# Kernel tuning notes

Hardware: AMD Instinct MI355X
Metric: run time of the kernel (lower is better)

The kernel has to match this reference:

```python
import jax, jax.numpy as jnp
import numpy as np

IN_BW = 4
W_BW = 4
EPS = 1e-5


def quantize(x, bw):
    # k-bit uniform quantizer on [-1, 1 - 2^(1-bw)] with straight-through rounding
    scale = 2.0 ** (bw - 1)
    xc = jnp.clip(x, -1.0, 1.0 - 1.0 / scale)
    q = jnp.round(xc * scale) / scale
    return xc + jax.lax.stop_gradient(q - xc)


def bconv(x, w, stride):
    # BinarizeConv2d: quantize activations (in_bw) and weights (weight_bw), then conv
    return jax.lax.conv_general_dilated(
        quantize(x, IN_BW), quantize(w, W_BW),
        window_strides=stride, padding='VALID',
        dimension_numbers=('NCHW', 'OIHW', 'NCHW'))


def bn2d(x, g, b):
    mean = x.mean(axis=(0, 2, 3), keepdims=True)
    var = x.var(axis=(0, 2, 3), keepdims=True)
    return (x - mean) * jax.lax.rsqrt(var + EPS) * g.reshape(1, -1, 1, 1) + b.reshape(1, -1, 1, 1)


def bn1d(x, g, b):
    mean = x.mean(axis=0, keepdims=True)
    var = x.var(axis=0, keepdims=True)
    return (x - mean) * jax.lax.rsqrt(var + EPS) * g + b


def htanh(x):
    return jnp.clip(x, -1.0, 1.0)


def setup_inputs() -> dict:
    key = jax.random.key(0)
    ks = jax.random.split(key, 24)
    B = 8192
    d = {'x': jax.random.normal(ks[0], (B, 1, 1250, 1), dtype=jnp.float32)}
    # conv weights OIHW
    shapes = [(3, 1, 6, 1), (5, 3, 5, 1), (10, 5, 4, 1), (20, 10, 4, 1), (20, 20, 4, 1)]
    for i, s in enumerate(shapes):
        d[f'w{i+1}'] = 0.3 * jax.random.normal(ks[1 + i], s, dtype=jnp.float32)
    d['fw1'] = 0.3 * jax.random.normal(ks[6], (10, 740), dtype=jnp.float32)
    d['fw2'] = 0.3 * jax.random.normal(ks[7], (2, 10), dtype=jnp.float32)
    chans = [3, 5, 10, 20, 20, 10, 2]
    for i, c in enumerate(chans):
        d[f'g{i+1}'] = 1.0 + 0.1 * jax.random.normal(ks[8 + i], (c,), dtype=jnp.float32)
        d[f'b{i+1}'] = 0.1 * jax.random.normal(ks[15 + i], (c,), dtype=jnp.float32)
    return d


def reference(x, w1, w2, w3, w4, w5, fw1, fw2,
              g1, g2, g3, g4, g5, g6, g7,
              b1, b2, b3, b4, b5, b6, b7):
    h = htanh(bn2d(bconv(x, w1, (2, 1)), g1, b1))
    h = htanh(bn2d(bconv(h, w2, (2, 1)), g2, b2))
    h = htanh(bn2d(bconv(h, w3, (2, 1)), g3, b3))
    h = htanh(bn2d(bconv(h, w4, (2, 1)), g4, b4))
    h = htanh(bn2d(bconv(h, w5, (2, 1)), g5, b5))
    h = h.reshape(h.shape[0], -1)  # (B, 20*37*1) = (B, 740)
    # dropout is identity in eval mode
    h = htanh(bn1d(quantize(h, IN_BW) @ quantize(fw1, W_BW).T, g6, b6))
    h = bn1d(quantize(h, IN_BW) @ quantize(fw2, W_BW).T, g7, b7)
    return h
```

## Files before the change

kernel.cpp:

```cpp
#include <hip/hip_runtime.h>

#define DEV __device__ __forceinline__

DEV float qwt(float w) {
    float y = fminf(fmaxf(w, -1.0f), 0.875f);
    return rintf(y * 8.0f) * 0.125f;
}
DEV int qw8i(float w) {
    float y = fminf(fmaxf(w, -1.0f), 0.875f);
    return (int)rintf(y * 8.0f);
}
DEV int q8i(float x, float a, float b) {
    float y = fmaf(x, a, b);
    y = fminf(fmaxf(y, -1.0f), 0.875f);
    return (int)rintf(y * 8.0f);
}
DEV float qact(float x, float a, float b) {
    float y = fmaf(x, a, b);
    y = fminf(fmaxf(y, -1.0f), 0.875f);
    return rintf(y * 8.0f) * 0.125f;
}

DEV int dot4(int a, int b, int c) {
#if __has_builtin(__builtin_amdgcn_sdot4)
    return __builtin_amdgcn_sdot4(a, b, c, false);
#else
    c += (int)(signed char)(a)       * (int)(signed char)(b);
    c += (int)(signed char)(a >> 8)  * (int)(signed char)(b >> 8);
    c += (int)(signed char)(a >> 16) * (int)(signed char)(b >> 16);
    c += (int)(signed char)(a >> 24) * (int)(signed char)(b >> 24);
    return c;
#endif
}
DEV unsigned alignpair(unsigned hi, unsigned lo, int bits) {
#if __has_builtin(__builtin_amdgcn_alignbit)
    return __builtin_amdgcn_alignbit(hi, lo, bits);
#else
    return bits ? ((lo >> bits) | (hi << (32 - bits))) : lo;
#endif
}

DEV void pack_layer(const float* w, int* o, int CIN, int COUT, int K, int t) {
    int KW = (K + 3) / 4;
    for (int i = t; i < COUT * CIN * KW; i += 256) {
        int j = i % KW, cc = i / KW;
        unsigned r = 0;
        for (int u = 0; u < 4; u++) {
            int k = 4 * j + u;
            int b = (k < K) ? (qw8i(w[cc * K + k]) & 0xff) : 0;
            r |= (unsigned)b << (8 * u);
        }
        o[i] = (int)r;
    }
}
__global__ __launch_bounds__(256) void pack_k(
    const float* w1, const float* w2, const float* w3, const float* w4, const float* w5,
    int* o1, int* o2, int* o3, int* o4, int* o5)
{
    int t = threadIdx.x;
    pack_layer(w1, o1, 1, 3, 6, t);
    pack_layer(w2, o2, 3, 5, 5, t);
    pack_layer(w3, o3, 5, 10, 4, t);
    pack_layer(w4, o4, 10, 20, 4, t);
    pack_layer(w5, o5, 20, 20, 4, t);
}

template<int CIN,int COUT,int K,int LINP,int LOUT,int LOUTP,int P,int R,bool IN_FLOAT,int LIN=0>
__global__ __launch_bounds__(256) void conv_k(
    const void* __restrict__ in_, const int* __restrict__ wqi,
    const float* __restrict__ tr, short* __restrict__ out,
    float* __restrict__ partial, int B)
{
    constexpr int KW   = (K + 3) / 4;
    constexpr int NE   = P + 2 * KW - 1;
    constexpr int ND   = (2 * (NE - 1) + 3) / 4 + 2;
    constexpr int LO_P = (LOUT + P - 1) / P;
    constexpr int GROUPS = R * LO_P;

    __shared__ __align__(16) signed char smem[R * CIN * LINP + 32];
    __shared__ float ts[CIN > 0 ? CIN : 1], tb[CIN > 0 ? CIN : 1];
    __shared__ float red[4][2 * COUT];

    const int tid = threadIdx.x;

    if constexpr (!IN_FLOAT) {
        if (tid < CIN) {
            ts[tid] = tr[tid] * 0.015625f;
            tb[tid] = tr[CIN + tid];
        }
        __syncthreads();
    }

    const int r0   = blockIdx.x * R;
    const int rcnt = min(R, B - r0);

    if constexpr (IN_FLOAT) {
        constexpr int CH = LIN / 2;
        const float2* gp = (const float2*)in_;
        for (int c = tid; c < rcnt * CH; c += 256) {
            int r = c / CH, rem = c - r * CH;
            float2 v = gp[(size_t)(r0 + r) * CH + rem];
            int b0 = q8i(v.x, 1.f, 0.f) & 0xff;
            int b1 = q8i(v.y, 1.f, 0.f) & 0xff;
            *(unsigned short*)(smem + r * LINP + rem * 2) =
                (unsigned short)(b0 | (b1 << 8));
        }
    } else {
        constexpr int CH  = CIN * LINP / 8;
        constexpr int CHC = LINP / 8;
        const int4* gp = (const int4*)((const short*)in_ + (size_t)r0 * CIN * LINP);
        for (int c = tid; c < rcnt * CH; c += 256) {
            int rem = c % CH;
            int ci = rem / CHC;
            float a = ts[ci], bo = tb[ci];
            int4 v = gp[c];
            int vs[4] = { v.x, v.y, v.z, v.w };
            unsigned pk[2];
#pragma unroll
            for (int u = 0; u < 2; u++) {
                unsigned pp = 0;
#pragma unroll
                for (int j = 0; j < 2; j++) {
                    int word = vs[u * 2 + j];
                    int b0 = q8i((float)(short)(word & 0xffff), a, bo) & 0xff;
                    int b1 = q8i((float)(short)(word >> 16),    a, bo) & 0xff;
                    pp |= (unsigned)(b0 | (b1 << 8)) << (16 * j);
                }
                pk[u] = pp;
            }
            ((uint2*)smem)[c] = make_uint2(pk[0], pk[1]);
        }
    }
    __syncthreads();

    float tsum[COUT], tsq[COUT];
#pragma unroll
    for (int c = 0; c < COUT; c++) { tsum[c] = 0.f; tsq[c] = 0.f; }

#pragma unroll 1
    for (int g = tid; g < GROUPS; g += 256) {
        int r = g / LO_P;
        if (r >= rcnt) continue;
        int l0   = (g - r * LO_P) * P;
        int pact = min(P, LOUT - l0);

        int acc[COUT][P];
#pragma unroll
        for (int co = 0; co < COUT; co++)
#pragma unroll
            for (int p = 0; p < P; p++) acc[co][p] = 0;

        const int ibase = r * CIN * LINP + 2 * l0;
        const int sh    = (P % 2 == 0) ? 0 : (ibase & 3);

        for (int ci = 0; ci < CIN; ci++) {
            const int* sp = (const int*)smem + ((ci * LINP + (ibase & ~3)) >> 2);
            int d[ND];
#pragma unroll
            for (int j = 0; j < ND; j++) d[j] = sp[j];
            int e[NE];
#pragma unroll
            for (int i = 0; i < NE; i++) {
                int off = sh + 2 * i;
                e[i] = (int)alignpair((unsigned)d[off / 4 + 1], (unsigned)d[off / 4], (off & 3) * 8);
            }
#pragma unroll
            for (int co = 0; co < COUT; co++) {
#pragma unroll
                for (int j = 0; j < KW; j++) {
                    int wv = wqi[(co * CIN + ci) * KW + j];
#pragma unroll
                    for (int p = 0; p < P; p++)
                        acc[co][p] = dot4(e[p + 2 * j], wv, acc[co][p]);
                }
            }
        }

        const size_t ob = (size_t)(r0 + r) * COUT * LOUTP + l0;
#pragma unroll
        for (int co = 0; co < COUT; co++) {
            if (pact == P) {
                short tmp[P];
#pragma unroll
                for (int p = 0; p < P; p++) {
                    tmp[p] = (short)acc[co][p];
                    float v = (float)acc[co][p] * 0.015625f;
                    tsum[co] += v;
                    tsq[co]   = fmaf(v, v, tsq[co]);
                }
                short* op = &out[ob + (size_t)co * LOUTP];
                if constexpr (P == 1) {
                    op[0] = tmp[0];
                } else if constexpr (P == 2) {
                    *(short2*)op = make_short2(tmp[0], tmp[1]);
                } else if constexpr (P == 4) {
                    *(short4*)op = make_short4(tmp[0], tmp[1], tmp[2], tmp[3]);
                } else if constexpr (P == 8) {
                    *(short4*)op       = make_short4(tmp[0], tmp[1], tmp[2], tmp[3]);
                    *(short4*)(op + 4) = make_short4(tmp[4], tmp[5], tmp[6], tmp[7]);
                }
            } else {
#pragma unroll
                for (int p = 0; p < P; p++) {
                    if (p < pact) {
                        out[ob + (size_t)co * LOUTP + p] = (short)acc[co][p];
                        float v = (float)acc[co][p] * 0.015625f;
                        tsum[co] += v;
                        tsq[co]   = fmaf(v, v, tsq[co]);
                    }
                }
            }
        }
    }

    const int lane = tid & 63, wid = tid >> 6;
#pragma unroll
    for (int co = 0; co < COUT; co++) {
        float s = tsum[co], q = tsq[co];
        for (int off = 32; off > 0; off >>= 1) {
            s += __shfl_down(s, off, 64);
            q += __shfl_down(q, off, 64);
        }
        if (lane == 0) { red[wid][2 * co] = s; red[wid][2 * co + 1] = q; }
    }
    __syncthreads();
    if (tid < 2 * COUT) {
        float v = red[0][tid] + red[1][tid] + red[2][tid] + red[3][tid];
        partial[(size_t)blockIdx.x * (2 * COUT) + tid] = v;
    }
}

__global__ __launch_bounds__(256) void finalize_k(
    const float* __restrict__ partial, int G, int C, double N,
    const float* __restrict__ gamma, const float* __restrict__ beta,
    float* __restrict__ trout)
{
    const int c = blockIdx.x;
    double s = 0.0, q = 0.0;
    for (int g = threadIdx.x; g < G; g += 256) {
        s += (double)partial[(size_t)g * 2 * C + 2 * c];
        q += (double)partial[(size_t)g * 2 * C + 2 * c + 1];
    }
    for (int off = 32; off > 0; off >>= 1) {
        s += __shfl_down(s, off, 64);
        q += __shfl_down(q, off, 64);
    }
    __shared__ double rs[4], rq[4];
    int lane = threadIdx.x & 63, wid = threadIdx.x >> 6;
    if (lane == 0) { rs[wid] = s; rq[wid] = q; }
    __syncthreads();
    if (threadIdx.x == 0) {
        double S = rs[0] + rs[1] + rs[2] + rs[3];
        double Q = rq[0] + rq[1] + rq[2] + rq[3];
        double mean = S / N;
        double var  = Q / N - mean * mean;
        double inv  = 1.0 / sqrt(var + 1e-5);
        double sc   = (double)gamma[c] * inv;
        trout[c]     = (float)sc;
        trout[C + c] = (float)((double)beta[c] - mean * sc);
    }
}

__global__ __launch_bounds__(256) void fc1_k(
    const short* __restrict__ y5, const float* __restrict__ fw1,
    const float* __restrict__ tr, float* __restrict__ z1,
    float* __restrict__ partial, int B)
{
    __shared__ float wq[7400];
    __shared__ float ts[20], tb[20];
    __shared__ float red[4][20];
    const int tid = threadIdx.x;
    for (int i = tid; i < 7400; i += 256) wq[i] = qwt(fw1[i]);
    if (tid < 20) { ts[tid] = tr[tid]; tb[tid] = tr[20 + tid]; }
    __syncthreads();

    const int lane = tid & 63, wid = tid >> 6;
    float tsum[10], tsq[10];
#pragma unroll
    for (int j = 0; j < 10; j++) { tsum[j] = 0.f; tsq[j] = 0.f; }

#pragma unroll 1
    for (int r = blockIdx.x * 4 + wid; r < B; r += gridDim.x * 4) {
        const short* xr = y5 + (size_t)r * 800;
        float acc[10];
#pragma unroll
        for (int j = 0; j < 10; j++) acc[j] = 0.f;
#pragma unroll 1
        for (int f = lane; f < 740; f += 64) {
            int c = f / 37, pos = f - c * 37;
            float x = qact((float)xr[c * 40 + pos] * 0.015625f, ts[c], tb[c]);
#pragma unroll
            for (int j = 0; j < 10; j++) acc[j] = fmaf(x, wq[j * 740 + f], acc[j]);
        }
#pragma unroll
        for (int j = 0; j < 10; j++) {
            float v = acc[j];
            for (int off = 1; off < 64; off <<= 1) v += __shfl_xor(v, off, 64);
            tsum[j] += v; tsq[j] = fmaf(v, v, tsq[j]);
            if (lane == j) z1[(size_t)r * 10 + j] = v;
        }
    }
    if (lane == 0) {
#pragma unroll
        for (int j = 0; j < 10; j++) { red[wid][2 * j] = tsum[j]; red[wid][2 * j + 1] = tsq[j]; }
    }
    __syncthreads();
    if (tid < 20) {
        float v = red[0][tid] + red[1][tid] + red[2][tid] + red[3][tid];
        partial[(size_t)blockIdx.x * 20 + tid] = v;
    }
}

__global__ __launch_bounds__(256) void fc2_fused_k(
    const float* __restrict__ z1, const float* __restrict__ fw2,
    const float* __restrict__ part6, int G6,
    const float* __restrict__ g6, const float* __restrict__ b6,
    const float* __restrict__ g7, const float* __restrict__ b7,
    float* __restrict__ outp, int B)
{
    __shared__ float zbuf[16384];
    __shared__ double dred[4][20];
    __shared__ double dtot[20];
    __shared__ float ts7[10], tb7[10], wq2[20];
    __shared__ float fr[4][4];
    __shared__ float tr8[4];

    const int tid = threadIdx.x;
    const int lane = tid & 63, wid = tid >> 6;

    double ls[20];
#pragma unroll
    for (int c = 0; c < 20; c++) ls[c] = 0.0;
    for (int g = tid; g < G6; g += 256) {
#pragma unroll
        for (int c = 0; c < 20; c++) ls[c] += (double)part6[(size_t)g * 20 + c];
    }
#pragma unroll
    for (int c = 0; c < 20; c++) {
        double v = ls[c];
        for (int off = 32; off > 0; off >>= 1) v += __shfl_down(v, off, 64);
        if (lane == 0) dred[wid][c] = v;
    }
    if (tid < 20) wq2[tid] = qwt(fw2[tid]);
    __syncthreads();
    if (tid < 20) dtot[tid] = dred[0][tid] + dred[1][tid] + dred[2][tid] + dred[3][tid];
    __syncthreads();
    if (tid < 10) {
        double N = (double)B;
        double mean = dtot[2 * tid] / N;
        double var  = dtot[2 * tid + 1] / N - mean * mean;
        double inv  = 1.0 / sqrt(var + 1e-5);
        double sc   = (double)g6[tid] * inv;
        ts7[tid] = (float)sc;
        tb7[tid] = (float)((double)b6[tid] - mean * sc);
    }
    __syncthreads();

    float s0 = 0.f, q0 = 0.f, s1 = 0.f, q1 = 0.f;
#pragma unroll 1
    for (int r = tid; r < B; r += 256) {
        float a0 = 0.f, a1 = 0.f;
#pragma unroll
        for (int i = 0; i < 10; i++) {
            float x = qact(z1[(size_t)r * 10 + i], ts7[i], tb7[i]);
            a0 = fmaf(x, wq2[i], a0);
            a1 = fmaf(x, wq2[10 + i], a1);
        }
        zbuf[r * 2]     = a0;
        zbuf[r * 2 + 1] = a1;
        s0 += a0; q0 = fmaf(a0, a0, q0);
        s1 += a1; q1 = fmaf(a1, a1, q1);
    }
    for (int off = 32; off > 0; off >>= 1) {
        s0 += __shfl_down(s0, off, 64); q0 += __shfl_down(q0, off, 64);
        s1 += __shfl_down(s1, off, 64); q1 += __shfl_down(q1, off, 64);
    }
    if (lane == 0) { fr[wid][0] = s0; fr[wid][1] = q0; fr[wid][2] = s1; fr[wid][3] = q1; }
    __syncthreads();
    if (tid < 2) {
        double S = 0.0, Q = 0.0;
        for (int w = 0; w < 4; w++) { S += (double)fr[w][2 * tid]; Q += (double)fr[w][2 * tid + 1]; }
        double N = (double)B;
        double mean = S / N;
        double var  = Q / N - mean * mean;
        double inv  = 1.0 / sqrt(var + 1e-5);
        double sc   = (double)g7[tid] * inv;
        tr8[tid]     = (float)sc;
        tr8[2 + tid] = (float)((double)b7[tid] - mean * sc);
    }
    __syncthreads();
    for (int i = tid; i < 2 * B; i += 256) {
        int c = i & 1;
        outp[i] = fmaf(zbuf[i], tr8[c], tr8[2 + c]);
    }
}

extern "C" void kernel_launch(void* const* d_in, const int* in_sizes, int n_in,
                              void* d_out, int out_size, void* d_ws, size_t ws_size,
                              hipStream_t stream)
{
    const float* x   = (const float*)d_in[0];
    const float* w1  = (const float*)d_in[1];
    const float* w2  = (const float*)d_in[2];
    const float* w3  = (const float*)d_in[3];
    const float* w4  = (const float*)d_in[4];
    const float* w5  = (const float*)d_in[5];
    const float* fw1 = (const float*)d_in[6];
    const float* fw2 = (const float*)d_in[7];
    const float *g[7], *bb[7];
    for (int i = 0; i < 7; i++) { g[i] = (const float*)d_in[8 + 2 * i]; bb[i] = (const float*)d_in[9 + 2 * i]; }

    char* ws = (char*)d_ws;
    size_t off = 0;
    auto alloc = [&](size_t bytes) -> void* {
        void* q = ws + off;
        off += (bytes + 255) & ~(size_t)255;
        return q;
    };
    short* y1 = (short*)alloc((size_t)8192 * 3 * 624 * 2);
    short* y2 = (short*)alloc((size_t)8192 * 5 * 312 * 2);
    short* y3 = (short*)alloc((size_t)8192 * 10 * 160 * 2);
    short* y4 = (short*)alloc((size_t)8192 * 20 * 80 * 2);
    short* y5 = (short*)alloc((size_t)8192 * 20 * 40 * 2);
    float* z1 = (float*)alloc((size_t)81920 * 4);
    float* partial = (float*)alloc((size_t)81920 * 4);
    int*   wp1 = (int*)alloc(64);   int* wp2 = (int*)alloc(256);
    int*   wp3 = (int*)alloc(256);  int* wp4 = (int*)alloc(1024);
    int*   wp5 = (int*)alloc(2048);
    float* tr2 = (float*)alloc(256); float* tr3 = (float*)alloc(256);
    float* tr4 = (float*)alloc(256); float* tr5 = (float*)alloc(256);
    float* tr6 = (float*)alloc(256); float* tr7 = (float*)alloc(256);

    const int B = 8192;

    pack_k<<<1, 256, 0, stream>>>(w1, w2, w3, w4, w5, wp1, wp2, wp3, wp4, wp5);

    {
        int grid = (B + 2) / 3;
        conv_k<1, 3, 6, 1252, 623, 624, 8, 3, true, 1250>
            <<<grid, 256, 0, stream>>>(x, wp1, nullptr, y1, partial, B);
        finalize_k<<<3, 256, 0, stream>>>(partial, grid, 3, (double)B * 623.0, g[0], bb[0], tr2);
    }
    {
        int grid = B / 4;
        conv_k<3, 5, 5, 624, 310, 312, 4, 4, false>
            <<<grid, 256, 0, stream>>>(y1, wp2, tr2, y2, partial, B);
        finalize_k<<<5, 256, 0, stream>>>(partial, grid, 5, (double)B * 310.0, g[1], bb[1], tr3);
    }
    {
        int grid = B / 4;
        conv_k<5, 10, 4, 312, 154, 160, 2, 4, false>
            <<<grid, 256, 0, stream>>>(y2, wp3, tr3, y3, partial, B);
        finalize_k<<<10, 256, 0, stream>>>(partial, grid, 10, (double)B * 154.0, g[2], bb[2], tr4);
    }
    {
        int grid = B / 4;
        conv_k<10, 20, 4, 160, 76, 80, 1, 4, false>
            <<<grid, 256, 0, stream>>>(y3, wp4, tr4, y4, partial, B);
        finalize_k<<<20, 256, 0, stream>>>(partial, grid, 20, (double)B * 76.0, g[3], bb[3], tr5);
    }
    {
        int grid = B / 8;
        conv_k<20, 20, 4, 80, 37, 40, 1, 8, false>
            <<<grid, 256, 0, stream>>>(y4, wp5, tr5, y5, partial, B);
        finalize_k<<<20, 256, 0, stream>>>(partial, grid, 20, (double)B * 37.0, g[4], bb[4], tr6);
    }
    {
        int grid = 2048;
        fc1_k<<<grid, 256, 0, stream>>>(y5, fw1, tr6, z1, partial, B);
        fc2_fused_k<<<1, 256, 0, stream>>>(z1, fw2, partial, grid,
                                           g[5], bb[5], g[6], bb[6],
                                           (float*)d_out, B);
    }
}
```

Measured before the change: 303.7 us.

## Fold BN stat finalization and weight packing into consumer kernels via integer atomics

Removes the separate finalize_k launches and the pack_k launch. Each conv or fc kernel now accumulates exact integer sums and sums of squares and adds them with 64-bit atomics into 64 slot buffers. The next kernel reduces those slots itself and computes the BN scale and shift at block start. The first conv packs its own weights into shared memory, and its block 0 packs the weights for the later layers. This cuts kernel launches and serial gaps, at the cost of atomics, a memset, and a small redundant stat reduction in every block.

```diff
diff --git a/kernel.cpp b/kernel.cpp
--- a/kernel.cpp
+++ b/kernel.cpp
@@ -39,6 +39,11 @@
     return bits ? ((lo >> bits) | (hi << (32 - bits))) : lo;
 #endif
 }
+DEV long long shfl_down_ll(long long v, int off) {
+    int lo = __shfl_down((int)(v & 0xffffffffll), off, 64);
+    int hi = __shfl_down((int)(v >> 32), off, 64);
+    return ((long long)hi << 32) | (unsigned)lo;
+}
 
 DEV void pack_layer(const float* w, int* o, int CIN, int COUT, int K, int t) {
     int KW = (K + 3) / 4;
@@ -53,23 +58,19 @@
         o[i] = (int)r;
     }
 }
-__global__ __launch_bounds__(256) void pack_k(
-    const float* w1, const float* w2, const float* w3, const float* w4, const float* w5,
-    int* o1, int* o2, int* o3, int* o4, int* o5)
-{
-    int t = threadIdx.x;
-    pack_layer(w1, o1, 1, 3, 6, t);
-    pack_layer(w2, o2, 3, 5, 5, t);
-    pack_layer(w3, o3, 5, 10, 4, t);
-    pack_layer(w4, o4, 10, 20, 4, t);
-    pack_layer(w5, o5, 20, 20, 4, t);
-}
 
 template<int CIN,int COUT,int K,int LINP,int LOUT,int LOUTP,int P,int R,bool IN_FLOAT,int LIN=0>
 __global__ __launch_bounds__(256) void conv_k(
     const void* __restrict__ in_, const int* __restrict__ wqi,
-    const float* __restrict__ tr, short* __restrict__ out,
-    float* __restrict__ partial, int B)
+    const long long* __restrict__ statsIn,
+    const float* __restrict__ gprev, const float* __restrict__ bprev,
+    double Nprev,
+    short* __restrict__ out, long long* __restrict__ statsOut, int B,
+    const float* __restrict__ wown,
+    const float* __restrict__ pw2, const float* __restrict__ pw3,
+    const float* __restrict__ pw4, const float* __restrict__ pw5,
+    int* __restrict__ owp2, int* __restrict__ owp3,
+    int* __restrict__ owp4, int* __restrict__ owp5)
 {
     constexpr int KW   = (K + 3) / 4;
     constexpr int NE   = P + 2 * KW - 1;
@@ -78,20 +79,60 @@
     constexpr int GROUPS = R * LO_P;
 
     __shared__ __align__(16) signed char smem[R * CIN * LINP + 32];
-    __shared__ float ts[CIN > 0 ? CIN : 1], tb[CIN > 0 ? CIN : 1];
-    __shared__ float red[4][2 * COUT];
+    __shared__ long long lred[2 * CIN * 16];
+    __shared__ long long redll[4][2 * COUT];
+    __shared__ float ts[CIN], tb[CIN];
+    __shared__ int lwq[IN_FLOAT ? (COUT * CIN * KW) : 1];
 
     const int tid = threadIdx.x;
-
-    if constexpr (!IN_FLOAT) {
+    const int bid = blockIdx.x;
+
+    if constexpr (IN_FLOAT) {
+        for (int i = tid; i < COUT * CIN * KW; i += 256) {
+            int j = i % KW, cc = i / KW;
+            unsigned rr = 0;
+            for (int u = 0; u < 4; u++) {
+                int k = 4 * j + u;
+                int bv = (k < K) ? (qw8i(wown[cc * K + k]) & 0xff) : 0;
+                rr |= (unsigned)bv << (8 * u);
+            }
+            lwq[i] = (int)rr;
+        }
+        if (bid == 0) {
+            pack_layer(pw2, owp2, 3, 5, 5, tid);
+            pack_layer(pw3, owp3, 5, 10, 4, tid);
+            pack_layer(pw4, owp4, 10, 20, 4, tid);
+            pack_layer(pw5, owp5, 20, 20, 4, tid);
+        }
+    } else {
+        for (int idx = tid; idx < 2 * CIN * 16; idx += 256) {
+            int ch = idx >> 4, si = idx & 15;
+            long long s = 0;
+#pragma unroll
+            for (int u = 0; u < 4; u++)
+                s += statsIn[(size_t)(si + 16 * u) * (2 * CIN) + ch];
+            lred[idx] = s;
+        }
+        __syncthreads();
         if (tid < CIN) {
-            ts[tid] = tr[tid] * 0.015625f;
-            tb[tid] = tr[CIN + tid];
+            long long Sk = 0, Sq = 0;
+#pragma unroll
+            for (int i = 0; i < 16; i++) {
+                Sk += lred[tid * 16 + i];
+                Sq += lred[(CIN + tid) * 16 + i];
+            }
+            double mean = (double)Sk / (64.0 * Nprev);
+            double ex2  = (double)Sq / (4096.0 * Nprev);
+            double var  = ex2 - mean * mean;
+            double inv  = 1.0 / sqrt(var + 1e-5);
+            double sc   = (double)gprev[tid] * inv;
+            ts[tid] = (float)sc * 0.015625f;
+            tb[tid] = (float)((double)bprev[tid] - mean * sc);
         }
         __syncthreads();
     }
 
-    const int r0   = blockIdx.x * R;
+    const int r0   = bid * R;
     const int rcnt = min(R, B - r0);
 
     if constexpr (IN_FLOAT) {
@@ -133,9 +174,9 @@
     }
     __syncthreads();
 
-    float tsum[COUT], tsq[COUT];
-#pragma unroll
-    for (int c = 0; c < COUT; c++) { tsum[c] = 0.f; tsq[c] = 0.f; }
+    int tsumK[COUT], tsqK[COUT];
+#pragma unroll
+    for (int c = 0; c < COUT; c++) { tsumK[c] = 0; tsqK[c] = 0; }
 
 #pragma unroll 1
     for (int g = tid; g < GROUPS; g += 256) {
@@ -168,7 +209,9 @@
             for (int co = 0; co < COUT; co++) {
 #pragma unroll
                 for (int j = 0; j < KW; j++) {
-                    int wv = wqi[(co * CIN + ci) * KW + j];
+                    int wv;
+                    if constexpr (IN_FLOAT) wv = lwq[(co * CIN + ci) * KW + j];
+                    else                    wv = wqi[(co * CIN + ci) * KW + j];
 #pragma unroll
                     for (int p = 0; p < P; p++)
                         acc[co][p] = dot4(e[p + 2 * j], wv, acc[co][p]);
@@ -183,10 +226,10 @@
                 short tmp[P];
 #pragma unroll
                 for (int p = 0; p < P; p++) {
-                    tmp[p] = (short)acc[co][p];
-                    float v = (float)acc[co][p] * 0.015625f;
-                    tsum[co] += v;
-                    tsq[co]   = fmaf(v, v, tsq[co]);
+                    int k = acc[co][p];
+                    tmp[p] = (short)k;
+                    tsumK[co] += k;
+                    tsqK[co]  += k * k;
                 }
                 short* op = &out[ob + (size_t)co * LOUTP];
                 if constexpr (P == 1) {
@@ -203,10 +246,10 @@
 #pragma unroll
                 for (int p = 0; p < P; p++) {
                     if (p < pact) {
-                        out[ob + (size_t)co * LOUTP + p] = (short)acc[co][p];
-                        float v = (float)acc[co][p] * 0.015625f;
-                        tsum[co] += v;
-                        tsq[co]   = fmaf(v, v, tsq[co]);
+                        int k = acc[co][p];
+                        out[ob + (size_t)co * LOUTP + p] = (short)k;
+                        tsumK[co] += k;
+                        tsqK[co]  += k * k;
                     }
                 }
             }
@@ -216,111 +259,110 @@
     const int lane = tid & 63, wid = tid >> 6;
 #pragma unroll
     for (int co = 0; co < COUT; co++) {
-        float s = tsum[co], q = tsq[co];
+        long long s = tsumK[co], q = tsqK[co];
         for (int off = 32; off > 0; off >>= 1) {
-            s += __shfl_down(s, off, 64);
-            q += __shfl_down(q, off, 64);
-        }
-        if (lane == 0) { red[wid][2 * co] = s; red[wid][2 * co + 1] = q; }
+            s += shfl_down_ll(s, off);
+            q += shfl_down_ll(q, off);
+        }
+        if (lane == 0) { redll[wid][co] = s; redll[wid][COUT + co] = q; }
     }
     __syncthreads();
     if (tid < 2 * COUT) {
-        float v = red[0][tid] + red[1][tid] + red[2][tid] + red[3][tid];
-        partial[(size_t)blockIdx.x * (2 * COUT) + tid] = v;
-    }
-}
-
-__global__ __launch_bounds__(256) void finalize_k(
-    const float* __restrict__ partial, int G, int C, double N,
-    const float* __restrict__ gamma, const float* __restrict__ beta,
-    float* __restrict__ trout)
-{
-    const int c = blockIdx.x;
-    double s = 0.0, q = 0.0;
-    for (int g = threadIdx.x; g < G; g += 256) {
-        s += (double)partial[(size_t)g * 2 * C + 2 * c];
-        q += (double)partial[(size_t)g * 2 * C + 2 * c + 1];
-    }
-    for (int off = 32; off > 0; off >>= 1) {
-        s += __shfl_down(s, off, 64);
-        q += __shfl_down(q, off, 64);
-    }
-    __shared__ double rs[4], rq[4];
-    int lane = threadIdx.x & 63, wid = threadIdx.x >> 6;
-    if (lane == 0) { rs[wid] = s; rq[wid] = q; }
-    __syncthreads();
-    if (threadIdx.x == 0) {
-        double S = rs[0] + rs[1] + rs[2] + rs[3];
-        double Q = rq[0] + rq[1] + rq[2] + rq[3];
-        double mean = S / N;
-        double var  = Q / N - mean * mean;
-        double inv  = 1.0 / sqrt(var + 1e-5);
-        double sc   = (double)gamma[c] * inv;
-        trout[c]     = (float)sc;
-        trout[C + c] = (float)((double)beta[c] - mean * sc);
+        long long v = redll[0][tid] + redll[1][tid] + redll[2][tid] + redll[3][tid];
+        atomicAdd((unsigned long long*)&statsOut[(size_t)(bid & 63) * (2 * COUT) + tid],
+                  (unsigned long long)v);
     }
 }
 
 __global__ __launch_bounds__(256) void fc1_k(
     const short* __restrict__ y5, const float* __restrict__ fw1,
-    const float* __restrict__ tr, float* __restrict__ z1,
-    float* __restrict__ partial, int B)
+    const long long* __restrict__ statsIn,
+    const float* __restrict__ g5, const float* __restrict__ b5,
+    float* __restrict__ z1, long long* __restrict__ statsOut, int B)
 {
     __shared__ float wq[7400];
     __shared__ float ts[20], tb[20];
-    __shared__ float red[4][20];
+    __shared__ long long lred[40 * 16];
+    __shared__ long long redS[4][10], redQ[4][10];
+
     const int tid = threadIdx.x;
+    const int bid = blockIdx.x;
+
+    for (int idx = tid; idx < 40 * 16; idx += 256) {
+        int ch = idx >> 4, si = idx & 15;
+        long long s = 0;
+#pragma unroll
+        for (int u = 0; u < 4; u++)
+            s += statsIn[(size_t)(si + 16 * u) * 40 + ch];
+        lred[idx] = s;
+    }
     for (int i = tid; i < 7400; i += 256) wq[i] = qwt(fw1[i]);
-    if (tid < 20) { ts[tid] = tr[tid]; tb[tid] = tr[20 + tid]; }
+    __syncthreads();
+    if (tid < 20) {
+        long long Sk = 0, Sq = 0;
+#pragma unroll
+        for (int i = 0; i < 16; i++) {
+            Sk += lred[tid * 16 + i];
+            Sq += lred[(20 + tid) * 16 + i];
+        }
+        double N = 8192.0 * 37.0;
+        double mean = (double)Sk / (64.0 * N);
+        double ex2  = (double)Sq / (4096.0 * N);
+        double var  = ex2 - mean * mean;
+        double inv  = 1.0 / sqrt(var + 1e-5);
+        double sc   = (double)g5[tid] * inv;
+        ts[tid] = (float)sc;
+        tb[tid] = (float)((double)b5[tid] - mean * sc);
+    }
     __syncthreads();
 
     const int lane = tid & 63, wid = tid >> 6;
-    float tsum[10], tsq[10];
-#pragma unroll
-    for (int j = 0; j < 10; j++) { tsum[j] = 0.f; tsq[j] = 0.f; }
-
+    const int r = bid * 4 + wid;
+    const short* xr = y5 + (size_t)r * 800;
+    float acc[10];
+#pragma unroll
+    for (int j = 0; j < 10; j++) acc[j] = 0.f;
 #pragma unroll 1
-    for (int r = blockIdx.x * 4 + wid; r < B; r += gridDim.x * 4) {
-        const short* xr = y5 + (size_t)r * 800;
-        float acc[10];
-#pragma unroll
-        for (int j = 0; j < 10; j++) acc[j] = 0.f;
-#pragma unroll 1
-        for (int f = lane; f < 740; f += 64) {
-            int c = f / 37, pos = f - c * 37;
-            float x = qact((float)xr[c * 40 + pos] * 0.015625f, ts[c], tb[c]);
-#pragma unroll
-            for (int j = 0; j < 10; j++) acc[j] = fmaf(x, wq[j * 740 + f], acc[j]);
-        }
-#pragma unroll
-        for (int j = 0; j < 10; j++) {
-            float v = acc[j];
-            for (int off = 1; off < 64; off <<= 1) v += __shfl_xor(v, off, 64);
-            tsum[j] += v; tsq[j] = fmaf(v, v, tsq[j]);
-            if (lane == j) z1[(size_t)r * 10 + j] = v;
-        }
+    for (int f = lane; f < 740; f += 64) {
+        int c = f / 37, pos = f - c * 37;
+        float x = qact((float)xr[c * 40 + pos] * 0.015625f, ts[c], tb[c]);
+#pragma unroll
+        for (int j = 0; j < 10; j++) acc[j] = fmaf(x, wq[j * 740 + f], acc[j]);
+    }
+    int tsumK[10]; long long tsqK[10];
+#pragma unroll
+    for (int j = 0; j < 10; j++) {
+        float v = acc[j];
+        for (int off = 1; off < 64; off <<= 1) v += __shfl_xor(v, off, 64);
+        if (lane == j) z1[(size_t)r * 10 + j] = v;
+        int kv = __float2int_rn(v * 64.0f);
+        tsumK[j] = kv;
+        tsqK[j]  = (long long)kv * kv;
     }
     if (lane == 0) {
 #pragma unroll
-        for (int j = 0; j < 10; j++) { red[wid][2 * j] = tsum[j]; red[wid][2 * j + 1] = tsq[j]; }
+        for (int j = 0; j < 10; j++) { redS[wid][j] = tsumK[j]; redQ[wid][j] = tsqK[j]; }
     }
     __syncthreads();
     if (tid < 20) {
-        float v = red[0][tid] + red[1][tid] + red[2][tid] + red[3][tid];
-        partial[(size_t)blockIdx.x * 20 + tid] = v;
+        int j = tid % 10;
+        long long v = (tid < 10)
+            ? (redS[0][j] + redS[1][j] + redS[2][j] + redS[3][j])
+            : (redQ[0][j] + redQ[1][j] + redQ[2][j] + redQ[3][j]);
+        atomicAdd((unsigned long long*)&statsOut[(size_t)(bid & 63) * 20 + tid],
+                  (unsigned long long)v);
     }
 }
 
 __global__ __launch_bounds__(256) void fc2_fused_k(
     const float* __restrict__ z1, const float* __restrict__ fw2,
-    const float* __restrict__ part6, int G6,
+    const long long* __restrict__ fc1slots,
     const float* __restrict__ g6, const float* __restrict__ b6,
     const float* __restrict__ g7, const float* __restrict__ b7,
     float* __restrict__ outp, int B)
 {
     __shared__ float zbuf[16384];
-    __shared__ double dred[4][20];
-    __shared__ double dtot[20];
+    __shared__ long long lred[20 * 16];
     __shared__ float ts7[10], tb7[10], wq2[20];
     __shared__ float fr[4][4];
     __shared__ float tr8[4];
@@ -328,27 +370,27 @@
     const int tid = threadIdx.x;
     const int lane = tid & 63, wid = tid >> 6;
 
-    double ls[20];
-#pragma unroll
-    for (int c = 0; c < 20; c++) ls[c] = 0.0;
-    for (int g = tid; g < G6; g += 256) {
-#pragma unroll
-        for (int c = 0; c < 20; c++) ls[c] += (double)part6[(size_t)g * 20 + c];
-    }
-#pragma unroll
-    for (int c = 0; c < 20; c++) {
-        double v = ls[c];
-        for (int off = 32; off > 0; off >>= 1) v += __shfl_down(v, off, 64);
-        if (lane == 0) dred[wid][c] = v;
+    for (int idx = tid; idx < 20 * 16; idx += 256) {
+        int ch = idx >> 4, si = idx & 15;
+        long long s = 0;
+#pragma unroll
+        for (int u = 0; u < 4; u++)
+            s += fc1slots[(size_t)(si + 16 * u) * 20 + ch];
+        lred[idx] = s;
     }
     if (tid < 20) wq2[tid] = qwt(fw2[tid]);
     __syncthreads();
-    if (tid < 20) dtot[tid] = dred[0][tid] + dred[1][tid] + dred[2][tid] + dred[3][tid];
-    __syncthreads();
     if (tid < 10) {
-        double N = (double)B;
-        double mean = dtot[2 * tid] / N;
-        double var  = dtot[2 * tid + 1] / N - mean * mean;
+        long long Sk = 0, Sq = 0;
+#pragma unroll
+        for (int i = 0; i < 16; i++) {
+            Sk += lred[tid * 16 + i];
+            Sq += lred[(10 + tid) * 16 + i];
+        }
+        double N = 8192.0;
+        double mean = (double)Sk / (64.0 * N);
+        double ex2  = (double)Sq / (4096.0 * N);
+        double var  = ex2 - mean * mean;
         double inv  = 1.0 / sqrt(var + 1e-5);
         double sc   = (double)g6[tid] * inv;
         ts7[tid] = (float)sc;
@@ -423,53 +465,36 @@
     short* y4 = (short*)alloc((size_t)8192 * 20 * 80 * 2);
     short* y5 = (short*)alloc((size_t)8192 * 20 * 40 * 2);
     float* z1 = (float*)alloc((size_t)81920 * 4);
-    float* partial = (float*)alloc((size_t)81920 * 4);
-    int*   wp1 = (int*)alloc(64);   int* wp2 = (int*)alloc(256);
-    int*   wp3 = (int*)alloc(256);  int* wp4 = (int*)alloc(1024);
-    int*   wp5 = (int*)alloc(2048);
-    float* tr2 = (float*)alloc(256); float* tr3 = (float*)alloc(256);
-    float* tr4 = (float*)alloc(256); float* tr5 = (float*)alloc(256);
-    float* tr6 = (float*)alloc(256); float* tr7 = (float*)alloc(256);
+    int*   wp2 = (int*)alloc(256);  int* wp3 = (int*)alloc(256);
+    int*   wp4 = (int*)alloc(1024); int* wp5 = (int*)alloc(2048);
+    long long* slots = (long long*)alloc((size_t)64 * 136 * 8);
+    long long* sl1 = slots;
+    long long* sl2 = sl1 + 64 * 6;
+    long long* sl3 = sl2 + 64 * 10;
+    long long* sl4 = sl3 + 64 * 20;
+    long long* sl5 = sl4 + 64 * 40;
+    long long* sl6 = sl5 + 64 * 40;
 
     const int B = 8192;
 
-    pack_k<<<1, 256, 0, stream>>>(w1, w2, w3, w4, w5, wp1, wp2, wp3, wp4, wp5);
-
-    {
-        int grid = (B + 2) / 3;
-        conv_k<1, 3, 6, 1252, 623, 624, 8, 3, true, 1250>
-            <<<grid, 256, 0, stream>>>(x, wp1, nullptr, y1, partial, B);
-        finalize_k<<<3, 256, 0, stream>>>(partial, grid, 3, (double)B * 623.0, g[0], bb[0], tr2);
-    }
-    {
-        int grid = B / 4;
-        conv_k<3, 5, 5, 624, 310, 312, 4, 4, false>
-            <<<grid, 256, 0, stream>>>(y1, wp2, tr2, y2, partial, B);
-        finalize_k<<<5, 256, 0, stream>>>(partial, grid, 5, (double)B * 310.0, g[1], bb[1], tr3);
-    }
-    {
-        int grid = B / 4;
-        conv_k<5, 10, 4, 312, 154, 160, 2, 4, false>
-            <<<grid, 256, 0, stream>>>(y2, wp3, tr3, y3, partial, B);
-        finalize_k<<<10, 256, 0, stream>>>(partial, grid, 10, (double)B * 154.0, g[2], bb[2], tr4);
-    }
-    {
-        int grid = B / 4;
-        conv_k<10, 20, 4, 160, 76, 80, 1, 4, false>
-            <<<grid, 256, 0, stream>>>(y3, wp4, tr4, y4, partial, B);
-        finalize_k<<<20, 256, 0, stream>>>(partial, grid, 20, (double)B * 76.0, g[3], bb[3], tr5);
-    }
-    {
-        int grid = B / 8;
-        conv_k<20, 20, 4, 80, 37, 40, 1, 8, false>
-            <<<grid, 256, 0, stream>>>(y4, wp5, tr5, y5, partial, B);
-        finalize_k<<<20, 256, 0, stream>>>(partial, grid, 20, (double)B * 37.0, g[4], bb[4], tr6);
-    }
-    {
-        int grid = 2048;
-        fc1_k<<<grid, 256, 0, stream>>>(y5, fw1, tr6, z1, partial, B);
-        fc2_fused_k<<<1, 256, 0, stream>>>(z1, fw2, partial, grid,
-                                           g[5], bb[5], g[6], bb[6],
-                                           (float*)d_out, B);
-    }
-}
+    hipMemsetAsync(slots, 0, (size_t)64 * 136 * 8, stream);
+
+    conv_k<1, 3, 6, 1252, 623, 624, 8, 3, true, 1250><<<2731, 256, 0, stream>>>(
+        x, nullptr, nullptr, nullptr, nullptr, 0.0, y1, sl1, B,
+        w1, w2, w3, w4, w5, wp2, wp3, wp4, wp5);
+    conv_k<3, 5, 5, 624, 310, 312, 4, 4, false><<<2048, 256, 0, stream>>>(
+        y1, wp2, sl1, g[0], bb[0], 8192.0 * 623.0, y2, sl2, B,
+        nullptr, nullptr, nullptr, nullptr, nullptr, nullptr, nullptr, nullptr, nullptr);
+    conv_k<5, 10, 4, 312, 154, 160, 2, 4, false><<<2048, 256, 0, stream>>>(
+        y2, wp3, sl2, g[1], bb[1], 8192.0 * 310.0, y3, sl3, B,
+        nullptr, nullptr, nullptr, nullptr, nullptr, nullptr, nullptr, nullptr, nullptr);
+    conv_k<10, 20, 4, 160, 76, 80, 1, 4, false><<<2048, 256, 0, stream>>>(
+        y3, wp4, sl3, g[2], bb[2], 8192.0 * 154.0, y4, sl4, B,
+        nullptr, nullptr, nullptr, nullptr, nullptr, nullptr, nullptr, nullptr, nullptr);
+    conv_k<20, 20, 4, 80, 37, 40, 1, 8, false><<<1024, 256, 0, stream>>>(
+        y4, wp5, sl4, g[3], bb[3], 8192.0 * 76.0, y5, sl5, B,
+        nullptr, nullptr, nullptr, nullptr, nullptr, nullptr, nullptr, nullptr, nullptr);
+    fc1_k<<<2048, 256, 0, stream>>>(y5, fw1, sl5, g[4], bb[4], z1, sl6, B);
+    fc2_fused_k<<<1, 256, 0, stream>>>(z1, fw2, sl6, g[5], bb[5], g[6], bb[6],
+                                       (float*)d_out, B);
+}
```

After: 384.0 us. 26.4% more time.
